# Kernel tuning notes

Measured on AMD Instinct MI355X. Metric: run time of the kernel, lower is better.

## Reference

```python
import jax, jax.numpy as jnp
import numpy as np


def _mha(q, k, v, num_heads):
    # q,k,v: [B, L, C] -> multi-head attention, scale = 1/sqrt(head_dim)
    B, Lq, C = q.shape
    Lk = k.shape[1]
    d = C // num_heads
    qh = q.reshape(B, Lq, num_heads, d)
    kh = k.reshape(B, Lk, num_heads, d)
    vh = v.reshape(B, Lk, num_heads, d)
    scale = 1.0 / jnp.sqrt(jnp.asarray(d, q.dtype))
    scores = jnp.einsum('blhd,bmhd->bhlm', qh, kh) * scale
    probs = jax.nn.softmax(scores, axis=-1)
    out = jnp.einsum('bhlm,bmhd->blhd', probs, vh)
    return out.reshape(B, Lq, C)


def setup_inputs() -> dict:
    key = jax.random.key(0)
    ks = jax.random.split(key, 9)
    b, n, f, l, C = 1, 4, 8, 256, 320
    s = 0.02
    return {
        'hidden_states': jax.random.normal(ks[0], (b * n * f, l, C), jnp.float32),
        'Wq': jax.random.normal(ks[1], (C, C), jnp.float32) * s,
        'Wk': jax.random.normal(ks[2], (C, C), jnp.float32) * s,
        'Wv': jax.random.normal(ks[3], (C, C), jnp.float32) * s,
        'Wo': jax.random.normal(ks[4], (C, C), jnp.float32) * s,
        'bo': jnp.zeros((C,), jnp.float32),
        'Wq_i2v': jax.random.normal(ks[5], (C, C), jnp.float32) * s,
        'Wo_i2v': jax.random.normal(ks[6], (C, C), jnp.float32) * s,
        'bo_i2v': jnp.zeros((C,), jnp.float32),
        'num_heads': 8,
        'num_views': 4,
        'num_frames': 8,
    }


def reference(hidden_states, Wq, Wk, Wv, Wo, bo, Wq_i2v, Wo_i2v, bo_i2v,
              num_heads, num_views, num_frames):
    BNF, l, C = hidden_states.shape
    n, f = num_views, num_frames
    b = BNF // (n * f)
    # '(b n f) l c -> (b f) (n l) c'
    h = hidden_states.reshape(b, n, f, l, C).transpose(0, 2, 1, 3, 4).reshape(b * f, n * l, C)
    L = n * l

    q = h @ Wq
    k = h @ Wk
    v = h @ Wv

    # first-frame KV broadcast across all frames within the same b
    k_first = jnp.broadcast_to(k.reshape(b, f, L, C)[:, 0:1], (b, f, L, C)).reshape(b * f, L, C)
    v_first = jnp.broadcast_to(v.reshape(b, f, L, C)[:, 0:1], (b, f, L, C)).reshape(b * f, L, C)

    base = _mha(q, k, v, num_heads)

    q_i2v = h @ Wq_i2v
    i2v = _mha(q_i2v, k_first, v_first, num_heads)
    i2v = i2v @ Wo_i2v + bo_i2v

    out = (base + i2v) @ Wo + bo

    # '(b f) (n l) c -> (b n f) l c'
    out = out.reshape(b, f, n, l, C).transpose(0, 2, 1, 3, 4).reshape(b * n * f, l, C)
    return out
```

## Files before the change

kernel.cpp:

```cpp
#include <hip/hip_runtime.h>
#include <hip/hip_bf16.h>

#define MROWS 8192
#define CDIM  320
#define QPAD  512

typedef __attribute__((ext_vector_type(8))) short bf16x8;
typedef __attribute__((ext_vector_type(4))) float f32x4;

__device__ __forceinline__ unsigned bfbits(float x) {
  union { float f; unsigned u; } a; a.f = x;
  return a.u + 0x8000u;
}
__device__ __forceinline__ void splitbf(float x, short& hi, short& lo) {
  unsigned hu = bfbits(x) & 0xffff0000u;
  union { unsigned u; float f; } h; h.u = hu;
  hi = (short)(hu >> 16);
  lo = (short)(bfbits(x - h.f) >> 16);
}
__device__ __forceinline__ unsigned pk_bf16(float a, float b) {
  union { __hip_bfloat162 h2; unsigned u; } cv;
  cv.h2 = __float22bfloat162_rn(float2{a, b});
  return cv.u;
}

__device__ __forceinline__ void cp16_g2l(const void* g, void* l) {
  __builtin_amdgcn_global_load_lds(
      (const __attribute__((address_space(1))) void*)g,
      (__attribute__((address_space(3))) void*)l, 16, 0, 0);
}

__device__ __forceinline__ int swizzle_row(int r) {
  int ff = r >> 10;
  int t  = r & 1023;
  int nn = t >> 8;
  int ll = t & 255;
  return nn * 2048 + ff * 256 + ll;
}

__global__ __launch_bounds__(256) void wc_kernel(
    const float* __restrict__ Woi, const float* __restrict__ Wo,
    float* __restrict__ Wc)
{
  const int r0 = blockIdx.x * 64, c0 = blockIdx.y * 64;
  __shared__ float As[64][36];
  __shared__ float Bs[32][68];
  const int tid = threadIdx.x, tx = tid & 15, ty = tid >> 4;
  float acc[4][4] = {};

  const int ra = tid >> 3, kq = (tid & 7) * 4;
  const int kb = tid >> 4, cq = (tid & 15) * 4;

  for (int k0 = 0; k0 < 320; k0 += 32) {
    float4 a1 = *(const float4*)(Woi + (size_t)(r0 + ra) * 320 + k0 + kq);
    float4 a2 = *(const float4*)(Woi + (size_t)(r0 + ra + 32) * 320 + k0 + kq);
    float4 b1 = *(const float4*)(Wo + (size_t)(k0 + kb) * 320 + c0 + cq);
    float4 b2 = *(const float4*)(Wo + (size_t)(k0 + kb + 16) * 320 + c0 + cq);
    __syncthreads();
    *(float4*)&As[ra][kq] = a1;
    *(float4*)&As[ra + 32][kq] = a2;
    *(float4*)&Bs[kb][cq] = b1;
    *(float4*)&Bs[kb + 16][cq] = b2;
    __syncthreads();
    #pragma unroll
    for (int kk = 0; kk < 32; ++kk) {
      float4 bv = *(const float4*)&Bs[kk][tx * 4];
      #pragma unroll
      for (int i = 0; i < 4; ++i) {
        float a = As[ty * 4 + i][kk];
        acc[i][0] = fmaf(a, bv.x, acc[i][0]);
        acc[i][1] = fmaf(a, bv.y, acc[i][1]);
        acc[i][2] = fmaf(a, bv.z, acc[i][2]);
        acc[i][3] = fmaf(a, bv.w, acc[i][3]);
      }
    }
  }
  #pragma unroll
  for (int i = 0; i < 4; ++i) {
    float4 v = make_float4(acc[i][0], acc[i][1], acc[i][2], acc[i][3]);
    *(float4*)(Wc + (size_t)(r0 + ty * 4 + i) * 320 + c0 + tx * 4) = v;
  }
}

__global__ __launch_bounds__(256) void pack_kernel(
    const float* __restrict__ hidden,
    const float* __restrict__ Wq, const float* __restrict__ Wk,
    const float* __restrict__ Wv, const float* __restrict__ Wqi,
    const float* __restrict__ Wo, const float* __restrict__ Wc,
    const float* __restrict__ bo, const float* __restrict__ boi,
    short* __restrict__ Ah, short* __restrict__ Al,
    short* __restrict__ WTh, short* __restrict__ WTl,
    short* __restrict__ WFh, short* __restrict__ WFl,
    float* __restrict__ bc,
    short* __restrict__ Qp, short* __restrict__ Kp, short* __restrict__ Qip,
    float qscale)
{
  const int b = blockIdx.x, tid = threadIdx.x;
  if (b < 64) {
    const int r0 = b * 128;
    for (int e = tid; e < 128 * 80; e += 256) {
      int r = e / 80, cq = (e % 80) * 4;
      float4 x = *(const float4*)(hidden + (size_t)swizzle_row(r0 + r) * 320 + cq);
      union { ushort4 v; short s[4]; } h, l;
      splitbf(x.x, h.s[0], l.s[0]); splitbf(x.y, h.s[1], l.s[1]);
      splitbf(x.z, h.s[2], l.s[2]); splitbf(x.w, h.s[3], l.s[3]);
      *(ushort4*)&Ah[(size_t)(r0 + r) * 320 + cq] = h.v;
      *(ushort4*)&Al[(size_t)(r0 + r) * 320 + cq] = l.v;
    }
  } else if (b < 128) {
    const int t2 = b - 64, wi = t2 >> 4, seg = t2 & 15;
    const float* W = wi == 0 ? Wq : wi == 1 ? Wk : wi == 2 ? Wv : Wqi;
    const float s = (wi == 0 || wi == 3) ? qscale : 1.0f;
    short* th = WTh + (size_t)wi * 320 * 320;
    short* tl = WTl + (size_t)wi * 320 * 320;
    for (int e = tid; e < 20 * 320; e += 256) {
      int n = seg * 20 + e / 320, k = e % 320;
      short hi, lo;
      splitbf(W[(size_t)k * 320 + n] * s, hi, lo);
      th[(size_t)n * 320 + k] = hi;
      tl[(size_t)n * 320 + k] = lo;
    }
  } else if (b < 160) {
    const int t2 = b - 128;
    for (int e = tid; e < 10 * 640; e += 256) {
      int n = t2 * 10 + e / 640, k = e % 640;
      float x = (k < 320) ? Wo[(size_t)k * 320 + n] : Wc[(size_t)(k - 320) * 320 + n];
      short hi, lo;
      splitbf(x, hi, lo);
      WFh[(size_t)n * 640 + k] = hi;
      WFl[(size_t)n * 640 + k] = lo;
    }
  } else if (b < 168) {
    const int n = (b - 160) * 40 + tid;
    if (tid < 40) {
      float s = bo[n];
      for (int j = 0; j < 320; ++j) s = fmaf(boi[j], Wo[(size_t)j * 320 + n], s);
      bc[n] = s;
    }
  } else {
    const int bz = b - 168, buf = bz >> 5, seg = bz & 31;
    short* P = buf == 0 ? Qp : buf == 1 ? Kp : Qip;
    const uint4 z = make_uint4(0, 0, 0, 0);
    for (int e = tid; e < 256 * 24; e += 256) {
      int row = (seg << 8) + (e / 24);
      int cc = e % 24, h = cc / 3, c3 = cc % 3;
      *(uint4*)&P[(size_t)row * QPAD + h * 64 + 40 + c3 * 8] = z;
    }
  }
}

template<int MT, int NT>
__global__ __launch_bounds__(256, 3) void mfma_gemm(
    const short* __restrict__ Ah, const short* __restrict__ Al,
    const short* __restrict__ BTh, const short* __restrict__ BTl,
    int K, int mode,
    short* __restrict__ Qp, short* __restrict__ Kp,
    short* __restrict__ Vt, short* __restrict__ Qip,
    float* __restrict__ Of, const float* __restrict__ bias)
{
  const int tid  = threadIdx.x;
  const int wave = tid >> 6;
  const int lane = tid & 63;
  const int quad = lane >> 4;
  const int l16  = lane & 15;
  const int row0 = blockIdx.x * (64 * MT);
  const int nbase = blockIdx.y * (16 * NT);

  __shared__ short Ash[64 * MT][32], Asl[64 * MT][32];
  __shared__ short Bsh[16 * NT][32], Bsl[16 * NT][32];

  f32x4 acc[MT][NT];
  #pragma unroll
  for (int mt = 0; mt < MT; ++mt)
    #pragma unroll
    for (int nt = 0; nt < NT; ++nt) acc[mt][nt] = (f32x4){0.f, 0.f, 0.f, 0.f};

  const int lr = lane >> 2, lc = (lane & 3) * 8;
  const short* gah = Ah + (size_t)(row0 + wave * 16 + lr) * K + lc;
  const short* gal = Al ? Al + (size_t)(row0 + wave * 16 + lr) * K + lc : nullptr;
  const short* gbh = BTh + (size_t)(nbase + wave * 16 + lr) * K + lc;
  const short* gbl = BTl + (size_t)(nbase + wave * 16 + lr) * K + lc;
  short* lah = &Ash[wave * 16][0];
  short* lal = &Asl[wave * 16][0];
  short* lbh = &Bsh[wave * 16][0];
  short* lbl = &Bsl[wave * 16][0];

  for (int k0 = 0; k0 < K; k0 += 32) {
    __syncthreads();
    #pragma unroll
    for (int s = 0; s < MT; ++s) {
      cp16_g2l(gah + (size_t)(s * 64) * K + k0, lah + s * 64 * 32);
      if (Al) cp16_g2l(gal + (size_t)(s * 64) * K + k0, lal + s * 64 * 32);
    }
    #pragma unroll
    for (int s = 0; s < NT / 4; ++s) {
      cp16_g2l(gbh + (size_t)(s * 64) * K + k0, lbh + s * 64 * 32);
      cp16_g2l(gbl + (size_t)(s * 64) * K + k0, lbl + s * 64 * 32);
    }
    __syncthreads();

    bf16x8 afh[MT], afl[MT], bfh[NT], bfl[NT];
    #pragma unroll
    for (int mt = 0; mt < MT; ++mt) {
      afh[mt] = *(const bf16x8*)&Ash[wave * (16 * MT) + mt * 16 + l16][quad * 8];
      if (Al) afl[mt] = *(const bf16x8*)&Asl[wave * (16 * MT) + mt * 16 + l16][quad * 8];
    }
    #pragma unroll
    for (int nt = 0; nt < NT; ++nt) {
      bfh[nt] = *(const bf16x8*)&Bsh[nt * 16 + l16][quad * 8];
      bfl[nt] = *(const bf16x8*)&Bsl[nt * 16 + l16][quad * 8];
    }
    #pragma unroll
    for (int mt = 0; mt < MT; ++mt)
      #pragma unroll
      for (int nt = 0; nt < NT; ++nt) {
        acc[mt][nt] = __builtin_amdgcn_mfma_f32_16x16x32_bf16(afh[mt], bfh[nt], acc[mt][nt], 0, 0, 0);
        acc[mt][nt] = __builtin_amdgcn_mfma_f32_16x16x32_bf16(afh[mt], bfl[nt], acc[mt][nt], 0, 0, 0);
        if (Al)
          acc[mt][nt] = __builtin_amdgcn_mfma_f32_16x16x32_bf16(afl[mt], bfh[nt], acc[mt][nt], 0, 0, 0);
      }
  }

  if (mode == 0) {
    #pragma unroll
    for (int mt = 0; mt < MT; ++mt)
      #pragma unroll
      for (int nt = 0; nt < NT; ++nt) {
        const int nn  = nbase + nt * 16 + l16;
        const int wi  = nn / 320;
        const int col = nn - wi * 320;
        const int rowb = row0 + wave * (16 * MT) + mt * 16 + quad * 4;
        if (wi == 2) {
          union { ushort4 v; short s[4]; } pk;
          #pragma unroll
          for (int r = 0; r < 4; ++r) pk.s[r] = (short)(bfbits(acc[mt][nt][r]) >> 16);
          *(ushort4*)&Vt[(size_t)col * MROWS + rowb] = pk.v;
        } else {
          short* Op = wi == 0 ? Qp : wi == 1 ? Kp : Qip;
          const int h    = col / 40;
          const int pcol = h * 64 + (col - h * 40);
          #pragma unroll
          for (int r = 0; r < 4; ++r)
            Op[(size_t)(rowb + r) * QPAD + pcol] = (short)(bfbits(acc[mt][nt][r]) >> 16);
        }
      }
  } else {
    #pragma unroll
    for (int mt = 0; mt < MT; ++mt)
      #pragma unroll
      for (int nt = 0; nt < NT; ++nt) {
        const int col  = nbase + nt * 16 + l16;
        const int rowb = row0 + wave * (16 * MT) + mt * 16 + quad * 4;
        const float bb = bias[col];
        #pragma unroll
        for (int r = 0; r < 4; ++r)
          Of[(size_t)swizzle_row(rowb + r) * CDIM + col] = acc[mt][nt][r] + bb;
      }
  }
}

__global__ __launch_bounds__(256, 4) void attn_kernel(
    const short* __restrict__ Qp, const short* __restrict__ Qip,
    const short* __restrict__ Kp, const short* __restrict__ Vtg,
    short* __restrict__ AOh)
{
  const int qblk = blockIdx.x;
  const int hh   = blockIdx.y;
  const int zz   = blockIdx.z;
  const int var  = zz >> 3;
  const int bf   = zz & 7;
  const int tid  = threadIdx.x;
  const int wave = tid >> 6;
  const int lane = tid & 63;
  const int quad = lane >> 4;
  const int l16  = lane & 15;

  const short* Q = var ? Qip : Qp;
  const int kvbase = var ? 0 : (bf << 10);
  const int coff = var * 320 + hh * 40;

  __shared__ short Ks[64][64];
  __shared__ short Vt[48][64];
  __shared__ short Ps[4][16][68];

  if (tid < 64) {
    const int pr = tid >> 3;
    uint4 fill = (pr == 0) ? make_uint4(0x3F803F80u, 0x3F803F80u, 0x3F803F80u, 0x3F803F80u)
                           : make_uint4(0, 0, 0, 0);
    *(uint4*)&Vt[40 + pr][(tid & 7) * 8] = fill;
  }

  bf16x8 qf0[2], qf1[2];
  #pragma unroll
  for (int qt = 0; qt < 2; ++qt) {
    const short* qp = Q + (size_t)((bf << 10) + (qblk << 7) + (wave << 5) + (qt << 4) + l16) * QPAD + hh * 64;
    qf0[qt] = *(const bf16x8*)(qp + quad * 8);
    qf1[qt] = *(const bf16x8*)(qp + 32 + quad * 8);
  }

  f32x4 acc[2][3];
  #pragma unroll
  for (int qt = 0; qt < 2; ++qt)
    #pragma unroll
    for (int t = 0; t < 3; ++t) acc[qt][t] = (f32x4){0.f, 0.f, 0.f, 0.f};

  const short* Kb = Kp + (size_t)kvbase * QPAD + hh * 64;
  const short* Vb = Vtg + (size_t)(hh * 40) * MROWS + kvbase;

  const int lrow = lane >> 3;
  const int gch  = ((lane & 7) ^ (lrow & 7)) * 8;
  const int sw   = l16 & 7;

  for (int s0 = 0; s0 < 1024; s0 += 64) {
    __syncthreads();
    #pragma unroll
    for (int j = 0; j < 4; ++j) {
      const int u = j * 4 + wave;
      if (u < 8) {
        cp16_g2l(Kb + (size_t)(s0 + u * 8 + lrow) * QPAD + gch, &Ks[u * 8][0]);
      } else if (u < 13) {
        cp16_g2l(Vb + (size_t)((u - 8) * 8 + lrow) * MROWS + s0 + gch, &Vt[(u - 8) * 8][0]);
      }
    }
    __syncthreads();

    bf16x8 vf[2][3];
    #pragma unroll
    for (int kh = 0; kh < 2; ++kh)
      #pragma unroll
      for (int t = 0; t < 3; ++t)
        vf[kh][t] = *(const bf16x8*)&Vt[t * 16 + l16][((kh * 4 + quad) ^ sw) * 8];

    #pragma unroll
    for (int qt = 0; qt < 2; ++qt) {
      #pragma unroll
      for (int kt = 0; kt < 4; ++kt) {
        const short* kr = &Ks[kt * 16 + l16][0];
        bf16x8 kb0 = *(const bf16x8*)(kr + (quad ^ sw) * 8);
        bf16x8 kb1 = *(const bf16x8*)(kr + ((quad + 4) ^ sw) * 8);
        f32x4 st = (f32x4){0.f, 0.f, 0.f, 0.f};
        st = __builtin_amdgcn_mfma_f32_16x16x32_bf16(kb0, qf0[qt], st, 0, 0, 0);
        st = __builtin_amdgcn_mfma_f32_16x16x32_bf16(kb1, qf1[qt], st, 0, 0, 0);
        float p0 = __builtin_amdgcn_exp2f(st[0]);
        float p1 = __builtin_amdgcn_exp2f(st[1]);
        float p2 = __builtin_amdgcn_exp2f(st[2]);
        float p3 = __builtin_amdgcn_exp2f(st[3]);
        uint2 pk;
        pk.x = pk_bf16(p0, p1);
        pk.y = pk_bf16(p2, p3);
        *(uint2*)&Ps[wave][l16][kt * 16 + quad * 4] = pk;
      }

      asm volatile("s_waitcnt lgkmcnt(0)" ::: "memory");

      bf16x8 pa0 = *(const bf16x8*)&Ps[wave][l16][quad * 8];
      bf16x8 pa1 = *(const bf16x8*)&Ps[wave][l16][32 + quad * 8];
      #pragma unroll
      for (int t = 0; t < 3; ++t) {
        acc[qt][t] = __builtin_amdgcn_mfma_f32_16x16x32_bf16(pa0, vf[0][t], acc[qt][t], 0, 0, 0);
        acc[qt][t] = __builtin_amdgcn_mfma_f32_16x16x32_bf16(pa1, vf[1][t], acc[qt][t], 0, 0, 0);
      }
    }
  }

  #pragma unroll
  for (int qt = 0; qt < 2; ++qt) {
    float invr[4];
    #pragma unroll
    for (int r = 0; r < 4; ++r) {
      float d = __shfl(acc[qt][2][r], quad * 16 + 8, 64);
      invr[r] = 1.f / d;
    }

    const int baserow = (bf << 10) + (qblk << 7) + (wave << 5) + (qt << 4) + quad * 4;
    #pragma unroll
    for (int t = 0; t < 3; ++t) {
      int dcol = t * 16 + l16;
      if (dcol < 40) {
        short* op = AOh + (size_t)baserow * 640 + coff + dcol;
        #pragma unroll
        for (int r = 0; r < 4; ++r)
          op[(size_t)r * 640] = (short)(bfbits(acc[qt][t][r] * invr[r]) >> 16);
      }
    }
  }
}

extern "C" void kernel_launch(void* const* d_in, const int* in_sizes, int n_in,
                              void* d_out, int out_size, void* d_ws, size_t ws_size,
                              hipStream_t stream) {
  const float* hidden  = (const float*)d_in[0];
  const float* Wq      = (const float*)d_in[1];
  const float* Wk      = (const float*)d_in[2];
  const float* Wv      = (const float*)d_in[3];
  const float* Wo      = (const float*)d_in[4];
  const float* bo      = (const float*)d_in[5];
  const float* Wq_i2v  = (const float*)d_in[6];
  const float* Wo_i2v  = (const float*)d_in[7];
  const float* bo_i2v  = (const float*)d_in[8];
  float* out = (float*)d_out;

  const size_t SZ  = (size_t)MROWS * CDIM;
  const size_t SZP = (size_t)MROWS * QPAD;
  short* Ah  = (short*)d_ws;
  short* Al  = Ah + SZ;
  short* AOh = Ah;
  short* Qp  = Al + SZ;
  short* Kp  = Qp + SZP;
  short* Qip = Kp + SZP;
  short* Vt  = Qip + SZP;
  short* WTh = Vt + (size_t)328 * MROWS;
  short* WTl = WTh + 409600;
  short* WFh = WTl + 409600;
  short* WFl = WFh + 204800;
  float* Wc  = (float*)(WFl + 204800);
  float* bc  = Wc + 102400;

  const float qscale = 0.22811011717177393f;

  wc_kernel<<<dim3(5, 5), 256, 0, stream>>>(Wo_i2v, Wo, Wc);

  pack_kernel<<<dim3(264), 256, 0, stream>>>(
      hidden, Wq, Wk, Wv, Wq_i2v, Wo, Wc, bo, bo_i2v,
      Ah, Al, WTh, WTl, WFh, WFl, bc, Qp, Kp, Qip, qscale);

  mfma_gemm<2, 8><<<dim3(64, 10), 256, 0, stream>>>(
      Ah, Al, WTh, WTl, 320, 0, Qp, Kp, Vt, Qip, nullptr, nullptr);

  attn_kernel<<<dim3(8, 8, 16), 256, 0, stream>>>(Qp, Qip, Kp, Vt, AOh);

  mfma_gemm<2, 4><<<dim3(64, 5), 256, 0, stream>>>(
      AOh, nullptr, WFh, WFl, 640, 1, nullptr, nullptr, nullptr, nullptr, out, bc);
}
```

Before: 202.6 us.

## Split attention work across eight waves with one query tile each

The attention kernel now launches 512 threads (8 waves) per block instead of 256, and each wave handles one 16-row query tile instead of two. The cooperative K/V tile load is spread over 8 waves, and the per-wave P scratch buffer is doubled. The aim is more latency hiding through higher wave count and less serial work per wave. The trade-off is that K/V fragments in LDS are reused by fewer query tiles per wave, and larger blocks may limit how many blocks fit on a CU.

```diff
diff --git a/kernel.cpp b/kernel.cpp
--- a/kernel.cpp
+++ b/kernel.cpp
@@ -259,7 +259,7 @@
   }
 }
 
-__global__ __launch_bounds__(256, 4) void attn_kernel(
+__global__ __launch_bounds__(512, 8) void attn_kernel(
     const short* __restrict__ Qp, const short* __restrict__ Qip,
     const short* __restrict__ Kp, const short* __restrict__ Vtg,
     short* __restrict__ AOh)
@@ -281,7 +281,7 @@
 
   __shared__ short Ks[64][64];
   __shared__ short Vt[48][64];
-  __shared__ short Ps[4][16][68];
+  __shared__ short Ps[8][16][68];
 
   if (tid < 64) {
     const int pr = tid >> 3;
@@ -290,19 +290,16 @@
     *(uint4*)&Vt[40 + pr][(tid & 7) * 8] = fill;
   }
 
-  bf16x8 qf0[2], qf1[2];
+  bf16x8 qf0, qf1;
+  {
+    const short* qp = Q + (size_t)((bf << 10) + (qblk << 7) + (wave << 4) + l16) * QPAD + hh * 64;
+    qf0 = *(const bf16x8*)(qp + quad * 8);
+    qf1 = *(const bf16x8*)(qp + 32 + quad * 8);
+  }
+
+  f32x4 acc[3];
   #pragma unroll
-  for (int qt = 0; qt < 2; ++qt) {
-    const short* qp = Q + (size_t)((bf << 10) + (qblk << 7) + (wave << 5) + (qt << 4) + l16) * QPAD + hh * 64;
-    qf0[qt] = *(const bf16x8*)(qp + quad * 8);
-    qf1[qt] = *(const bf16x8*)(qp + 32 + quad * 8);
-  }
-
-  f32x4 acc[2][3];
-  #pragma unroll
-  for (int qt = 0; qt < 2; ++qt)
-    #pragma unroll
-    for (int t = 0; t < 3; ++t) acc[qt][t] = (f32x4){0.f, 0.f, 0.f, 0.f};
+  for (int t = 0; t < 3; ++t) acc[t] = (f32x4){0.f, 0.f, 0.f, 0.f};
 
   const short* Kb = Kp + (size_t)kvbase * QPAD + hh * 64;
   const short* Vb = Vtg + (size_t)(hh * 40) * MROWS + kvbase;
@@ -314,8 +311,8 @@
   for (int s0 = 0; s0 < 1024; s0 += 64) {
     __syncthreads();
     #pragma unroll
-    for (int j = 0; j < 4; ++j) {
-      const int u = j * 4 + wave;
+    for (int j = 0; j < 2; ++j) {
+      const int u = j * 8 + wave;
       if (u < 8) {
         cp16_g2l(Kb + (size_t)(s0 + u * 8 + lrow) * QPAD + gch, &Ks[u * 8][0]);
       } else if (u < 13) {
@@ -332,56 +329,50 @@
         vf[kh][t] = *(const bf16x8*)&Vt[t * 16 + l16][((kh * 4 + quad) ^ sw) * 8];
 
     #pragma unroll
-    for (int qt = 0; qt < 2; ++qt) {
-      #pragma unroll
-      for (int kt = 0; kt < 4; ++kt) {
-        const short* kr = &Ks[kt * 16 + l16][0];
-        bf16x8 kb0 = *(const bf16x8*)(kr + (quad ^ sw) * 8);
-        bf16x8 kb1 = *(const bf16x8*)(kr + ((quad + 4) ^ sw) * 8);
-        f32x4 st = (f32x4){0.f, 0.f, 0.f, 0.f};
-        st = __builtin_amdgcn_mfma_f32_16x16x32_bf16(kb0, qf0[qt], st, 0, 0, 0);
-        st = __builtin_amdgcn_mfma_f32_16x16x32_bf16(kb1, qf1[qt], st, 0, 0, 0);
-        float p0 = __builtin_amdgcn_exp2f(st[0]);
-        float p1 = __builtin_amdgcn_exp2f(st[1]);
-        float p2 = __builtin_amdgcn_exp2f(st[2]);
-        float p3 = __builtin_amdgcn_exp2f(st[3]);
-        uint2 pk;
-        pk.x = pk_bf16(p0, p1);
-        pk.y = pk_bf16(p2, p3);
-        *(uint2*)&Ps[wave][l16][kt * 16 + quad * 4] = pk;
-      }
-
-      asm volatile("s_waitcnt lgkmcnt(0)" ::: "memory");
-
-      bf16x8 pa0 = *(const bf16x8*)&Ps[wave][l16][quad * 8];
-      bf16x8 pa1 = *(const bf16x8*)&Ps[wave][l16][32 + quad * 8];
-      #pragma unroll
-      for (int t = 0; t < 3; ++t) {
-        acc[qt][t] = __builtin_amdgcn_mfma_f32_16x16x32_bf16(pa0, vf[0][t], acc[qt][t], 0, 0, 0);
-        acc[qt][t] = __builtin_amdgcn_mfma_f32_16x16x32_bf16(pa1, vf[1][t], acc[qt][t], 0, 0, 0);
-      }
-    }
-  }
-
+    for (int kt = 0; kt < 4; ++kt) {
+      const short* kr = &Ks[kt * 16 + l16][0];
+      bf16x8 kb0 = *(const bf16x8*)(kr + (quad ^ sw) * 8);
+      bf16x8 kb1 = *(const bf16x8*)(kr + ((quad + 4) ^ sw) * 8);
+      f32x4 st = (f32x4){0.f, 0.f, 0.f, 0.f};
+      st = __builtin_amdgcn_mfma_f32_16x16x32_bf16(kb0, qf0, st, 0, 0, 0);
+      st = __builtin_amdgcn_mfma_f32_16x16x32_bf16(kb1, qf1, st, 0, 0, 0);
+      float p0 = __builtin_amdgcn_exp2f(st[0]);
+      float p1 = __builtin_amdgcn_exp2f(st[1]);
+      float p2 = __builtin_amdgcn_exp2f(st[2]);
+      float p3 = __builtin_amdgcn_exp2f(st[3]);
+      uint2 pk;
+      pk.x = pk_bf16(p0, p1);
+      pk.y = pk_bf16(p2, p3);
+      *(uint2*)&Ps[wave][l16][kt * 16 + quad * 4] = pk;
+    }
+
+    asm volatile("s_waitcnt lgkmcnt(0)" ::: "memory");
+
+    bf16x8 pa0 = *(const bf16x8*)&Ps[wave][l16][quad * 8];
+    bf16x8 pa1 = *(const bf16x8*)&Ps[wave][l16][32 + quad * 8];
+    #pragma unroll
+    for (int t = 0; t < 3; ++t) {
+      acc[t] = __builtin_amdgcn_mfma_f32_16x16x32_bf16(pa0, vf[0][t], acc[t], 0, 0, 0);
+      acc[t] = __builtin_amdgcn_mfma_f32_16x16x32_bf16(pa1, vf[1][t], acc[t], 0, 0, 0);
+    }
+  }
+
+  float invr[4];
   #pragma unroll
-  for (int qt = 0; qt < 2; ++qt) {
-    float invr[4];
-    #pragma unroll
-    for (int r = 0; r < 4; ++r) {
-      float d = __shfl(acc[qt][2][r], quad * 16 + 8, 64);
-      invr[r] = 1.f / d;
-    }
-
-    const int baserow = (bf << 10) + (qblk << 7) + (wave << 5) + (qt << 4) + quad * 4;
-    #pragma unroll
-    for (int t = 0; t < 3; ++t) {
-      int dcol = t * 16 + l16;
-      if (dcol < 40) {
-        short* op = AOh + (size_t)baserow * 640 + coff + dcol;
-        #pragma unroll
-        for (int r = 0; r < 4; ++r)
-          op[(size_t)r * 640] = (short)(bfbits(acc[qt][t][r] * invr[r]) >> 16);
-      }
+  for (int r = 0; r < 4; ++r) {
+    float d = __shfl(acc[2][r], quad * 16 + 8, 64);
+    invr[r] = 1.f / d;
+  }
+
+  const int baserow = (bf << 10) + (qblk << 7) + (wave << 4) + quad * 4;
+  #pragma unroll
+  for (int t = 0; t < 3; ++t) {
+    int dcol = t * 16 + l16;
+    if (dcol < 40) {
+      short* op = AOh + (size_t)baserow * 640 + coff + dcol;
+      #pragma unroll
+      for (int r = 0; r < 4; ++r)
+        op[(size_t)r * 640] = (short)(bfbits(acc[t][r] * invr[r]) >> 16);
     }
   }
 }
@@ -427,7 +418,7 @@
   mfma_gemm<2, 8><<<dim3(64, 10), 256, 0, stream>>>(
       Ah, Al, WTh, WTl, 320, 0, Qp, Kp, Vt, Qip, nullptr, nullptr);
 
-  attn_kernel<<<dim3(8, 8, 16), 256, 0, stream>>>(Qp, Qip, Kp, Vt, AOh);
+  attn_kernel<<<dim3(8, 8, 16), 512, 0, stream>>>(Qp, Qip, Kp, Vt, AOh);
 
   mfma_gemm<2, 4><<<dim3(64, 5), 256, 0, stream>>>(
       AOh, nullptr, WFh, WFl, 640, 1, nullptr, nullptr, nullptr, nullptr, out, bc);
```

Result: faster. 198.3 us (-2.1%).
